# Optimization experiments

Measured on AMD Instinct MI355X. Metric: run time of the kernel, lower is better.

Reference implementation:

```python
import jax, jax.numpy as jnp
import numpy as np

DIM = 256
H = 4
D = DIM // H  # head_dim = 64
SCALE = D ** -0.5


def setup_inputs() -> dict:
    key = jax.random.key(0)
    ks = jax.random.split(key, 12)
    B, N, M = 4, 2048, 2048
    x_query = jax.random.normal(ks[0], (B, N, DIM), dtype=jnp.float32)
    x_context = jax.random.normal(ks[1], (B, M, DIM), dtype=jnp.float32)
    geo_bias = jax.random.normal(ks[2], (B, H, N, M), dtype=jnp.float32)
    init = 1.0 / np.sqrt(DIM)
    Wq = jax.random.uniform(ks[3], (DIM, DIM), jnp.float32, -init, init)
    bq = jax.random.uniform(ks[4], (DIM,), jnp.float32, -init, init)
    Wk = jax.random.uniform(ks[5], (DIM, DIM), jnp.float32, -init, init)
    bk = jax.random.uniform(ks[6], (DIM,), jnp.float32, -init, init)
    Wv = jax.random.uniform(ks[7], (DIM, DIM), jnp.float32, -init, init)
    bv = jax.random.uniform(ks[8], (DIM,), jnp.float32, -init, init)
    Wo = jax.random.uniform(ks[9], (DIM, DIM), jnp.float32, -init, init)
    bo = jax.random.uniform(ks[10], (DIM,), jnp.float32, -init, init)
    return {"x_query": x_query, "x_context": x_context, "geo_bias": geo_bias,
            "Wq": Wq, "bq": bq, "Wk": Wk, "bk": bk, "Wv": Wv, "bv": bv,
            "Wo": Wo, "bo": bo}


def reference(x_query, x_context, geo_bias, Wq, bq, Wk, bk, Wv, bv, Wo, bo):
    B, N, _ = x_query.shape
    M = x_context.shape[1]
    # projections; nn.Linear computes x @ W.T + b
    q = (x_query @ Wq.T + bq).reshape(B, N, H, D).transpose(0, 2, 1, 3)   # (B,H,N,D)
    k = (x_context @ Wk.T + bk).reshape(B, M, H, D).transpose(0, 2, 1, 3)  # (B,H,M,D)
    v = (x_context @ Wv.T + bv).reshape(B, M, H, D).transpose(0, 2, 1, 3)  # (B,H,M,D)
    attn = jnp.einsum("bhnd,bhmd->bhnm", q, k) * SCALE + geo_bias
    attn = jax.nn.softmax(attn, axis=-1)
    out = jnp.einsum("bhnm,bhmd->bhnd", attn, v)
    out = out.transpose(0, 2, 1, 3).reshape(B, N, DIM)
    return out @ Wo.T + bo
```

## Files before the change

kernel.cpp:

```cpp
#include <hip/hip_runtime.h>

typedef unsigned short u16;
typedef unsigned int u32;
using bf16x8  = __attribute__((ext_vector_type(8))) __bf16;
using u16x8   = __attribute__((ext_vector_type(8), may_alias)) u16;
using u16x4   = __attribute__((ext_vector_type(4), may_alias)) u16;
using f32x4   = __attribute__((ext_vector_type(4))) float;
using f32x4_a = __attribute__((ext_vector_type(4), may_alias)) float;

#define DEV __device__ __forceinline__

constexpr int Bn = 4, Hn = 4, Nn = 2048, Mn = 2048, Dn = 64, DIMn = 256;
constexpr float SCALEc = 0.125f;
constexpr float SHIFTc = 12.0f;

DEV float bf2f(u16 h) { u32 u = ((u32)h) << 16; return __builtin_bit_cast(float, u); }
DEV u16 f2bf(float f) {
    u32 u = __builtin_bit_cast(u32, f);
    u += 0x7fffu + ((u >> 16) & 1u);
    return (u16)(u >> 16);
}
DEV bf16x8 ld8bf(const u16* p) {
    return __builtin_bit_cast(bf16x8, *reinterpret_cast<const u16x8*>(p));
}
DEV bf16x8 ld8f_bf(const float* p) {
    const f32x4 a = *reinterpret_cast<const f32x4_a*>(p);
    const f32x4 b = *reinterpret_cast<const f32x4_a*>(p + 4);
    u16x8 r;
    r[0] = f2bf(a[0]); r[1] = f2bf(a[1]); r[2] = f2bf(a[2]); r[3] = f2bf(a[3]);
    r[4] = f2bf(b[0]); r[5] = f2bf(b[1]); r[6] = f2bf(b[2]); r[7] = f2bf(b[3]);
    return __builtin_bit_cast(bf16x8, r);
}

__global__ __launch_bounds__(256) void qproj_kernel(
    const float* __restrict__ X, const float* __restrict__ W,
    const float* __restrict__ bias, float* __restrict__ Q)
{
    const int row0 = blockIdx.x * 32;
    const int wave = threadIdx.x >> 6, lane = threadIdx.x & 63;
    const int quad = lane >> 4, l16 = lane & 15;
    const int o0 = wave * 64;
    const int b = row0 >> 11, n0 = row0 & 2047;

    f32x4 acc[2][4] = {};
    #pragma unroll
    for (int k0 = 0; k0 < 256; k0 += 32) {
        bf16x8 af[2], wf[4];
        #pragma unroll
        for (int ns = 0; ns < 2; ns++)
            af[ns] = ld8f_bf(X + (size_t)(row0 + ns * 16 + l16) * DIMn + k0 + quad * 8);
        #pragma unroll
        for (int os = 0; os < 4; os++)
            wf[os] = ld8f_bf(W + (size_t)(o0 + os * 16 + l16) * DIMn + k0 + quad * 8);
        #pragma unroll
        for (int ns = 0; ns < 2; ns++)
            #pragma unroll
            for (int os = 0; os < 4; os++)
                acc[ns][os] = __builtin_amdgcn_mfma_f32_16x16x32_bf16(af[ns], wf[os], acc[ns][os], 0, 0, 0);
    }
    #pragma unroll
    for (int os = 0; os < 4; os++) {
        const int col = o0 + os * 16 + l16;
        const int h = col >> 6, d = col & 63;
        const float bb = bias[col];
        #pragma unroll
        for (int ns = 0; ns < 2; ns++)
            #pragma unroll
            for (int r = 0; r < 4; r++) {
                const int n = n0 + ns * 16 + quad * 4 + r;
                Q[((size_t)(b * Hn + h) * Nn + n) * Dn + d] = acc[ns][os][r] + bb;
            }
    }
}

__global__ __launch_bounds__(256) void kvproj_kernel(
    const float* __restrict__ X,
    const float* __restrict__ Wk, const float* __restrict__ bk,
    const float* __restrict__ Wv, const float* __restrict__ bv,
    u16* __restrict__ K, u16* __restrict__ V)
{
    const int row0 = blockIdx.x * 32;
    const int wave = threadIdx.x >> 6, lane = threadIdx.x & 63;
    const int quad = lane >> 4, l16 = lane & 15;
    const int o0 = wave * 64;
    const int b = row0 >> 11, n0 = row0 & 2047;

    f32x4 ack[2][4] = {};
    f32x4 acv[4][2] = {};
    #pragma unroll
    for (int k0 = 0; k0 < 256; k0 += 32) {
        bf16x8 af[2], wkf[4], wvf[4];
        #pragma unroll
        for (int ns = 0; ns < 2; ns++)
            af[ns] = ld8f_bf(X + (size_t)(row0 + ns * 16 + l16) * DIMn + k0 + quad * 8);
        #pragma unroll
        for (int os = 0; os < 4; os++) {
            wkf[os] = ld8f_bf(Wk + (size_t)(o0 + os * 16 + l16) * DIMn + k0 + quad * 8);
            wvf[os] = ld8f_bf(Wv + (size_t)(o0 + os * 16 + l16) * DIMn + k0 + quad * 8);
        }
        #pragma unroll
        for (int ns = 0; ns < 2; ns++)
            #pragma unroll
            for (int os = 0; os < 4; os++) {
                ack[ns][os] = __builtin_amdgcn_mfma_f32_16x16x32_bf16(af[ns], wkf[os], ack[ns][os], 0, 0, 0);
                acv[os][ns] = __builtin_amdgcn_mfma_f32_16x16x32_bf16(wvf[os], af[ns], acv[os][ns], 0, 0, 0);
            }
    }
    #pragma unroll
    for (int os = 0; os < 4; os++) {
        const int col = o0 + os * 16 + l16;
        const int h = col >> 6, d = col & 63;
        const float bb = bk[col];
        #pragma unroll
        for (int ns = 0; ns < 2; ns++)
            #pragma unroll
            for (int r = 0; r < 4; r++) {
                const int m = n0 + ns * 16 + quad * 4 + r;
                K[((size_t)(b * Hn + h) * Mn + m) * Dn + d] = f2bf(ack[ns][os][r] + bb);
            }
    }
    #pragma unroll
    for (int os = 0; os < 4; os++)
        #pragma unroll
        for (int r = 0; r < 4; r++) {
            const int colf = o0 + os * 16 + quad * 4 + r;
            const int h = colf >> 6, d = colf & 63;
            const float bb = bv[colf];
            #pragma unroll
            for (int ns = 0; ns < 2; ns++) {
                const int m = n0 + ns * 16 + l16;
                V[((size_t)(b * Hn + h) * Dn + d) * Mn + m] = f2bf(acv[os][ns][r] + bb);
            }
        }
}

__global__ __launch_bounds__(256) void attn_kernel(
    const float* __restrict__ Q,
    const u16* __restrict__ K,
    const u16* __restrict__ V,
    const float* __restrict__ geo,
    u16* __restrict__ AO)
{
    __shared__ __align__(16) u16 lds[4][2][16 * 144];

    const int h = blockIdx.y, b = blockIdx.z;
    const int wave = threadIdx.x >> 6, lane = threadIdx.x & 63;
    const int quad = lane >> 4, l16 = lane & 15;
    const int nbase = blockIdx.x * 64 + wave * 16;

    const float* Qh = Q + ((size_t)(b * Hn + h) * Nn + nbase) * Dn;
    const u16*   Kh = K + (size_t)(b * Hn + h) * Mn * Dn;
    const u16*   Vh = V + (size_t)(b * Hn + h) * Dn * Mn;
    const float* Gl = geo + ((size_t)(b * Hn + h) * Nn + nbase + l16) * (size_t)Mn;

    bf16x8 qh[2], ql[2];
    #pragma unroll
    for (int kh = 0; kh < 2; kh++) {
        const float* qp = Qh + (size_t)l16 * Dn + kh * 32 + quad * 8;
        const f32x4 a = *reinterpret_cast<const f32x4_a*>(qp);
        const f32x4 c = *reinterpret_cast<const f32x4_a*>(qp + 4);
        u16x8 hi, lo;
        #pragma unroll
        for (int j = 0; j < 4; j++) {
            hi[j] = f2bf(a[j]); lo[j] = f2bf(a[j] - bf2f(hi[j]));
            hi[4 + j] = f2bf(c[j]); lo[4 + j] = f2bf(c[j] - bf2f(hi[4 + j]));
        }
        qh[kh] = __builtin_bit_cast(bf16x8, hi);
        ql[kh] = __builtin_bit_cast(bf16x8, lo);
    }

    f32x4 oacc[4] = {};
    float lsum = 0.f;

    for (int m0 = 0; m0 < Mn; m0 += 128) {
        u16* pl = &lds[wave][(m0 >> 7) & 1][0];
        #pragma unroll
        for (int ms = 0; ms < 8; ms++) {
            const int mb = m0 + ms * 16;
            const u16* kp = Kh + (size_t)(mb + l16) * Dn + quad * 8;
            const bf16x8 kb0 = ld8bf(kp);
            const bf16x8 kb1 = ld8bf(kp + 32);
            f32x4 s = {};
            s = __builtin_amdgcn_mfma_f32_16x16x32_bf16(kb0, qh[0], s, 0, 0, 0);
            s = __builtin_amdgcn_mfma_f32_16x16x32_bf16(kb0, ql[0], s, 0, 0, 0);
            s = __builtin_amdgcn_mfma_f32_16x16x32_bf16(kb1, qh[1], s, 0, 0, 0);
            s = __builtin_amdgcn_mfma_f32_16x16x32_bf16(kb1, ql[1], s, 0, 0, 0);
            const f32x4 g = *reinterpret_cast<const f32x4_a*>(Gl + mb + quad * 4);
            u16x4 pk;
            float ls = 0.f;
            #pragma unroll
            for (int r = 0; r < 4; r++) {
                const float p = __expf(fmaf(s[r], SCALEc, g[r]) - SHIFTc);
                ls += p;
                pk[r] = f2bf(p);
            }
            lsum += ls;
            *reinterpret_cast<u16x4*>(pl + l16 * 144 + ms * 16 + quad * 4) = pk;
        }
        #pragma unroll
        for (int kh = 0; kh < 4; kh++) {
            const bf16x8 pa = ld8bf(pl + l16 * 144 + kh * 32 + quad * 8);
            #pragma unroll
            for (int ds = 0; ds < 4; ds++) {
                const bf16x8 vb = ld8bf(Vh + (size_t)(ds * 16 + l16) * Mn + m0 + kh * 32 + quad * 8);
                oacc[ds] = __builtin_amdgcn_mfma_f32_16x16x32_bf16(pa, vb, oacc[ds], 0, 0, 0);
            }
        }
    }

    lsum += __shfl_xor(lsum, 16);
    lsum += __shfl_xor(lsum, 32);

    u16* AOr = AO + ((size_t)b * Nn + nbase) * DIMn + h * Dn;
    #pragma unroll
    for (int r = 0; r < 4; r++) {
        const float inv = 1.0f / __shfl(lsum, quad * 4 + r);
        #pragma unroll
        for (int ds = 0; ds < 4; ds++)
            AOr[(size_t)(quad * 4 + r) * DIMn + ds * 16 + l16] = f2bf(oacc[ds][r] * inv);
    }
}

__global__ __launch_bounds__(256) void oproj_kernel(
    const u16* __restrict__ A, const float* __restrict__ W,
    const float* __restrict__ bias, float* __restrict__ out)
{
    const int row0 = blockIdx.x * 32;
    const int wave = threadIdx.x >> 6, lane = threadIdx.x & 63;
    const int quad = lane >> 4, l16 = lane & 15;
    const int o0 = wave * 64;

    f32x4 acc[2][4] = {};
    #pragma unroll
    for (int k0 = 0; k0 < 256; k0 += 32) {
        bf16x8 af[2], wf[4];
        #pragma unroll
        for (int ns = 0; ns < 2; ns++)
            af[ns] = ld8bf(A + (size_t)(row0 + ns * 16 + l16) * DIMn + k0 + quad * 8);
        #pragma unroll
        for (int os = 0; os < 4; os++)
            wf[os] = ld8f_bf(W + (size_t)(o0 + os * 16 + l16) * DIMn + k0 + quad * 8);
        #pragma unroll
        for (int ns = 0; ns < 2; ns++)
            #pragma unroll
            for (int os = 0; os < 4; os++)
                acc[ns][os] = __builtin_amdgcn_mfma_f32_16x16x32_bf16(af[ns], wf[os], acc[ns][os], 0, 0, 0);
    }
    #pragma unroll
    for (int os = 0; os < 4; os++) {
        const int col = o0 + os * 16 + l16;
        const float bb = bias[col];
        #pragma unroll
        for (int ns = 0; ns < 2; ns++)
            #pragma unroll
            for (int r = 0; r < 4; r++) {
                const int row = row0 + ns * 16 + quad * 4 + r;
                out[(size_t)row * DIMn + col] = acc[ns][os][r] + bb;
            }
    }
}

extern "C" void kernel_launch(void* const* d_in, const int* in_sizes, int n_in,
                              void* d_out, int out_size, void* d_ws, size_t ws_size,
                              hipStream_t stream) {
    const float* xq  = (const float*)d_in[0];
    const float* xc  = (const float*)d_in[1];
    const float* geo = (const float*)d_in[2];
    const float* Wq  = (const float*)d_in[3];
    const float* bq  = (const float*)d_in[4];
    const float* Wk  = (const float*)d_in[5];
    const float* bk  = (const float*)d_in[6];
    const float* Wv  = (const float*)d_in[7];
    const float* bv  = (const float*)d_in[8];
    const float* Wo  = (const float*)d_in[9];
    const float* bo  = (const float*)d_in[10];

    char* ws = (char*)d_ws;
    float* Qw  = (float*)ws;
    u16*   Kw  = (u16*)(ws + 8388608);
    u16*   Vw  = (u16*)(ws + 8388608 + 4194304);
    u16*   AOw = (u16*)(ws + 8388608 + 2 * 4194304);

    qproj_kernel<<<256, 256, 0, stream>>>(xq, Wq, bq, Qw);
    kvproj_kernel<<<256, 256, 0, stream>>>(xc, Wk, bk, Wv, bv, Kw, Vw);
    attn_kernel<<<dim3(Nn / 64, Hn, Bn), 256, 0, stream>>>(Qw, Kw, Vw, geo, AOw);
    oproj_kernel<<<256, 256, 0, stream>>>(AOw, Wo, bo, (float*)d_out);
}
```

Baseline: 583.1 us.

## Split attention over key dimension with separate combine kernel

Splits the key/context range into S chunks (four when the workspace is large enough), so the attention grid grows fourfold. Each block writes unnormalized fp32 partial outputs and row sums, and a new combine kernel adds them, normalizes and writes bf16. This targets low occupancy from the original 512-block grid. It costs extra global traffic for the fp32 partials, one more kernel launch, and a fallback path with S=1 that still pays for the combine. The LDS row stride also changes from 144 to 152 and double buffering is dropped.

```diff
diff --git a/kernel.cpp b/kernel.cpp
--- a/kernel.cpp
+++ b/kernel.cpp
@@ -13,6 +13,7 @@
 constexpr int Bn = 4, Hn = 4, Nn = 2048, Mn = 2048, Dn = 64, DIMn = 256;
 constexpr float SCALEc = 0.125f;
 constexpr float SHIFTc = 12.0f;
+constexpr int LSTRIDE = 152;
 
 DEV float bf2f(u16 h) { u32 u = ((u32)h) << 16; return __builtin_bit_cast(float, u); }
 DEV u16 f2bf(float f) {
@@ -139,14 +140,18 @@
     const u16* __restrict__ K,
     const u16* __restrict__ V,
     const float* __restrict__ geo,
-    u16* __restrict__ AO)
-{
-    __shared__ __align__(16) u16 lds[4][2][16 * 144];
-
-    const int h = blockIdx.y, b = blockIdx.z;
+    float* __restrict__ Pnum,
+    float* __restrict__ Lsum,
+    int S)
+{
+    __shared__ __align__(16) u16 lds[4][16 * LSTRIDE];
+
+    const int h = blockIdx.y;
+    const int b = blockIdx.z / S, split = blockIdx.z % S;
     const int wave = threadIdx.x >> 6, lane = threadIdx.x & 63;
     const int quad = lane >> 4, l16 = lane & 15;
     const int nbase = blockIdx.x * 64 + wave * 16;
+    const int mlen = Mn / S, mbeg = split * mlen;
 
     const float* Qh = Q + ((size_t)(b * Hn + h) * Nn + nbase) * Dn;
     const u16*   Kh = K + (size_t)(b * Hn + h) * Mn * Dn;
@@ -171,9 +176,9 @@
 
     f32x4 oacc[4] = {};
     float lsum = 0.f;
-
-    for (int m0 = 0; m0 < Mn; m0 += 128) {
-        u16* pl = &lds[wave][(m0 >> 7) & 1][0];
+    u16* pl = &lds[wave][0];
+
+    for (int m0 = mbeg; m0 < mbeg + mlen; m0 += 128) {
         #pragma unroll
         for (int ms = 0; ms < 8; ms++) {
             const int mb = m0 + ms * 16;
@@ -195,14 +200,14 @@
                 pk[r] = f2bf(p);
             }
             lsum += ls;
-            *reinterpret_cast<u16x4*>(pl + l16 * 144 + ms * 16 + quad * 4) = pk;
+            *reinterpret_cast<u16x4*>(pl + l16 * LSTRIDE + ms * 16 + quad * 4) = pk;
         }
         #pragma unroll
         for (int kh = 0; kh < 4; kh++) {
-            const bf16x8 pa = ld8bf(pl + l16 * 144 + kh * 32 + quad * 8);
+            const bf16x8 pa = ld8bf(pl + l16 * LSTRIDE + kh * 32 + quad * 8);
             #pragma unroll
             for (int ds = 0; ds < 4; ds++) {
-                const bf16x8 vb = ld8bf(Vh + (size_t)(ds * 16 + l16) * Mn + m0 + kh * 32 + quad * 8);
+                const bf16x8 vb = ld8bf(Vh + (size_t)(ds * 16 + l16) * Mn + (m0 - mbeg) + mbeg + kh * 32 + quad * 8);
                 oacc[ds] = __builtin_amdgcn_mfma_f32_16x16x32_bf16(pa, vb, oacc[ds], 0, 0, 0);
             }
         }
@@ -211,14 +216,45 @@
     lsum += __shfl_xor(lsum, 16);
     lsum += __shfl_xor(lsum, 32);
 
-    u16* AOr = AO + ((size_t)b * Nn + nbase) * DIMn + h * Dn;
-    #pragma unroll
-    for (int r = 0; r < 4; r++) {
-        const float inv = 1.0f / __shfl(lsum, quad * 4 + r);
+    float* PN = Pnum + (size_t)split * (Bn * (size_t)Nn * DIMn)
+                     + ((size_t)b * Nn + nbase) * DIMn + h * Dn;
+    #pragma unroll
+    for (int r = 0; r < 4; r++)
         #pragma unroll
         for (int ds = 0; ds < 4; ds++)
-            AOr[(size_t)(quad * 4 + r) * DIMn + ds * 16 + l16] = f2bf(oacc[ds][r] * inv);
-    }
+            PN[(size_t)(quad * 4 + r) * DIMn + ds * 16 + l16] = oacc[ds][r];
+
+    if (lane < 16)
+        Lsum[(((size_t)split * Bn + b) * Hn + h) * Nn + nbase + l16] = lsum;
+}
+
+__global__ __launch_bounds__(256) void combine_kernel(
+    const float* __restrict__ Pnum, const float* __restrict__ Lsum,
+    u16* __restrict__ AO, int S)
+{
+    const int idx = blockIdx.x * 256 + threadIdx.x;
+    const int row = idx >> 5;
+    const int c0  = (idx & 31) * 8;
+    const int b = row >> 11, n = row & 2047, h = c0 >> 6;
+
+    float l = 0.f;
+    for (int s = 0; s < S; s++)
+        l += Lsum[(((size_t)s * Bn + b) * Hn + h) * Nn + n];
+    const float inv = 1.0f / l;
+
+    f32x4 a0 = {}, a1 = {};
+    for (int s = 0; s < S; s++) {
+        const float* p = Pnum + (size_t)s * (Bn * (size_t)Nn * DIMn) + (size_t)row * DIMn + c0;
+        a0 += *reinterpret_cast<const f32x4_a*>(p);
+        a1 += *reinterpret_cast<const f32x4_a*>(p + 4);
+    }
+    u16x8 o;
+    #pragma unroll
+    for (int j = 0; j < 4; j++) {
+        o[j]     = f2bf(a0[j] * inv);
+        o[4 + j] = f2bf(a1[j] * inv);
+    }
+    *reinterpret_cast<u16x8*>(AO + (size_t)row * DIMn + c0) = o;
 }
 
 __global__ __launch_bounds__(256) void oproj_kernel(
@@ -275,14 +311,19 @@
     const float* Wo  = (const float*)d_in[9];
     const float* bo  = (const float*)d_in[10];
 
+    const int S = (ws_size >= (60ull << 20)) ? 4 : 1;
+
     char* ws = (char*)d_ws;
-    float* Qw  = (float*)ws;
-    u16*   Kw  = (u16*)(ws + 8388608);
-    u16*   Vw  = (u16*)(ws + 8388608 + 4194304);
-    u16*   AOw = (u16*)(ws + 8388608 + 2 * 4194304);
+    float* Qw   = (float*)ws;
+    u16*   Kw   = (u16*)(ws + (8ull << 20));
+    u16*   Vw   = (u16*)(ws + (12ull << 20));
+    u16*   AOw  = (u16*)(ws + (16ull << 20));
+    float* Pnum = (float*)(ws + (20ull << 20));
+    float* Lsum = (float*)(ws + (20ull << 20) + (size_t)S * (8ull << 20));
 
     qproj_kernel<<<256, 256, 0, stream>>>(xq, Wq, bq, Qw);
     kvproj_kernel<<<256, 256, 0, stream>>>(xc, Wk, bk, Wv, bv, Kw, Vw);
-    attn_kernel<<<dim3(Nn / 64, Hn, Bn), 256, 0, stream>>>(Qw, Kw, Vw, geo, AOw);
+    attn_kernel<<<dim3(Nn / 64, Hn, Bn * S), 256, 0, stream>>>(Qw, Kw, Vw, geo, Pnum, Lsum, S);
+    combine_kernel<<<(Bn * Nn * 32) / 256, 256, 0, stream>>>(Pnum, Lsum, AOw, S);
     oproj_kernel<<<256, 256, 0, stream>>>(AOw, Wo, bo, (float*)d_out);
 }
```

Measured after the change: 556.3 us. 4.6% less time.
